# Performance work log

Hardware: AMD Instinct MI355X
Metric: run time of the kernel (lower is better)

## Reference

```python
import jax, jax.numpy as jnp
import numpy as np

PRE_NMS_THRESH = 0.05
PRE_NMS_TOP_N = 1000
NMS_THRESH = 0.6
FPN_POST_NMS_TOP_N = 100
MIN_SIZE = 0
OFFSET = 10000.0  # per-class coordinate offset for batched per-class NMS
NEG = -1e9


def bilinear_resize(x, out_h, out_w):
    # x: [H, W, C] -> [out_h, out_w, C], matches torch interpolate(align_corners=False)
    H, W, _ = x.shape
    def grid(in_size, out_size):
        scale = in_size / out_size
        src = (jnp.arange(out_size, dtype=jnp.float32) + 0.5) * scale - 0.5
        src = jnp.clip(src, 0.0, in_size - 1.0)
        i0 = jnp.floor(src).astype(jnp.int32)
        i1 = jnp.minimum(i0 + 1, in_size - 1)
        lam = src - i0.astype(jnp.float32)
        return i0, i1, lam
    r0, r1, rl = grid(H, out_h)
    c0, c1, cl = grid(W, out_w)
    x = x[r0] * (1.0 - rl)[:, None, None] + x[r1] * rl[:, None, None]
    x = x[:, c0] * (1.0 - cl)[None, :, None] + x[:, c1] * cl[None, :, None]
    return x


def box_iou_plus1(b):
    area = (b[:, 2] - b[:, 0] + 1.0) * (b[:, 3] - b[:, 1] + 1.0)
    lt = jnp.maximum(b[:, None, :2], b[None, :, :2])
    rb = jnp.minimum(b[:, None, 2:], b[None, :, 2:])
    wh = jnp.clip(rb - lt + 1.0, 0.0)
    inter = wh[..., 0] * wh[..., 1]
    union = area[:, None] + area[None, :] - inter
    return inter / jnp.maximum(union, 1e-6)


def _forward(locations, box_cls, box_regression, centerness, box_mask, h, w):
    N, C, H, W = box_cls.shape
    M2 = box_mask.shape[1]
    Mi = int(np.sqrt(M2))
    HW = H * W
    K = PRE_NMS_TOP_N

    cls = jax.nn.sigmoid(box_cls.transpose(0, 2, 3, 1).reshape(N, HW, C))
    reg = box_regression.transpose(0, 2, 3, 1).reshape(N, HW, 4)
    cent = jax.nn.sigmoid(centerness.reshape(N, HW))
    mask = jax.nn.sigmoid(box_mask.transpose(0, 2, 3, 1))  # [N,H,W,M2]

    cand = cls > PRE_NMS_THRESH               # candidates from raw cls scores
    scr = cls * cent[:, :, None]              # centerness-weighted scores

    def per_image(cand_i, scr_i, reg_i, mask_i):
        # --- threshold + per-image topk (fixed K, padded with NEG) ---
        flat = jnp.where(cand_i, scr_i, NEG).reshape(HW * C)
        vals, idx = jax.lax.top_k(flat, K)
        valid = vals > NEG / 2
        loc_idx = idx // C
        labels = idx % C + 1                  # 1-based class labels
        locs = locations[loc_idx]             # [K,2]
        r = reg_i[loc_idx]                    # [K,4]
        boxes = jnp.stack([locs[:, 0] - r[:, 0], locs[:, 1] - r[:, 1],
                           locs[:, 0] + r[:, 2], locs[:, 1] + r[:, 3]], axis=1)
        scores = jnp.sqrt(jnp.where(valid, vals, 1.0)) * valid

        # --- mask paste: mean of upsampled mask over (buggy) box region ---
        up = bilinear_resize(mask_i, h, w)                      # [h,w,M2]
        integ = jnp.pad(jnp.cumsum(jnp.cumsum(up, 0), 1), ((1, 0), (1, 0), (0, 0)))
        bi = boxes.astype(jnp.int32)          # torch .int() truncation
        x1 = jnp.maximum(bi[:, 0], 0); x2 = jnp.minimum(bi[:, 2], h - 1)
        y1 = jnp.maximum(bi[:, 1], 0); y2 = jnp.minimum(bi[:, 3], w - 1)
        # original skip condition is (x1>=x2 or y1>=x2) -- bug replicated; extra
        # y1<y2 guard avoids NaN mean over empty region
        region_ok = (x1 < x2) & (y1 < x2) & (y1 < y2)
        x1c = jnp.clip(x1, 0, h); x2c = jnp.clip(x2, 0, h)
        y1c = jnp.clip(y1, 0, w); y2c = jnp.clip(y2, 0, w)
        s = integ[x2c, y2c] - integ[x1c, y2c] - integ[x2c, y1c] + integ[x1c, y1c]
        area = jnp.maximum((x2c - x1c) * (y2c - y1c), 1).astype(s.dtype)
        prob = ((s / area[:, None]) * region_ok[:, None]).reshape(K, Mi, Mi)

        # --- clip_to_image (x in [0,w-1], y in [0,h-1]) + remove_small_boxes ---
        bx = jnp.stack([jnp.clip(boxes[:, 0], 0, w - 1), jnp.clip(boxes[:, 1], 0, h - 1),
                        jnp.clip(boxes[:, 2], 0, w - 1), jnp.clip(boxes[:, 3], 0, h - 1)], 1)
        ws_ = bx[:, 2] - bx[:, 0] + 1.0
        hs_ = bx[:, 3] - bx[:, 1] + 1.0
        valid = valid & (ws_ >= MIN_SIZE) & (hs_ >= MIN_SIZE)

        # --- per-class greedy NMS via class-offset trick (fixed shape) ---
        nb = bx + (labels.astype(bx.dtype) * OFFSET)[:, None]
        order = jnp.argsort(-jnp.where(valid, scores, -1.0))
        nb_s, sc_s, v_s = nb[order], scores[order], valid[order]
        iou = box_iou_plus1(nb_s)
        rng = jnp.arange(K)
        def step(keep, i):
            ki = keep[i] & v_s[i]
            keep = keep.at[i].set(ki)
            keep = keep & ~(ki & (iou[i] > NMS_THRESH) & (rng > i))
            return keep, None
        keep, _ = jax.lax.scan(step, jnp.ones(K, bool), jnp.arange(K))
        v_final = keep & v_s

        # --- keep fpn_post_nms_top_n highest-scoring survivors ---
        fvals, fidx = jax.lax.top_k(jnp.where(v_final, sc_s, -1.0), FPN_POST_NMS_TOP_N)
        sel = order[fidx]
        vfin = v_final[fidx]
        return (bx[sel], scores[sel] * vfin, labels[sel], prob[sel] * vfin[:, None, None], vfin)

    return jax.vmap(per_image)(cand, scr, reg, mask)


def setup_inputs() -> dict:
    key = jax.random.key(0)
    ks = jax.random.split(key, 4)
    N, C, H, W, M2 = 2, 80, 32, 40, 196
    stride = 8
    ys, xs = jnp.meshgrid(jnp.arange(H), jnp.arange(W), indexing='ij')
    locations = jnp.stack([xs.reshape(-1), ys.reshape(-1)], 1).astype(jnp.float32) * stride + stride // 2
    box_cls = jax.random.normal(ks[0], (N, C, H, W), jnp.float32) - 2.0
    box_regression = jax.random.uniform(ks[1], (N, 4, H, W), jnp.float32) * 60.0 + 4.0
    centerness = jax.random.normal(ks[2], (N, 1, H, W), jnp.float32)
    box_mask = jax.random.normal(ks[3], (N, M2, H, W), jnp.float32)
    return {"locations": locations, "box_cls": box_cls, "box_regression": box_regression,
            "centerness": centerness, "box_mask": box_mask, "image_h": 256, "image_w": 320}


def reference(locations, box_cls, box_regression, centerness, box_mask, image_h, image_w):
    return _forward(locations, box_cls, box_regression, centerness, box_mask, image_h, image_w)
```

## Files before the change

### kernel.cpp

```cpp
#include <hip/hip_runtime.h>

#define DEVI __device__ __forceinline__

constexpr int N_ = 2, C_ = 80, H_ = 32, W_ = 40, HW_ = H_ * W_, HWC_ = HW_ * C_;
constexpr int KTOP = 1000, M2_ = 196;
constexpr int IMH = 256, IMW = 320;
constexpr int BUFCAP = 4096;
constexpr int NB = 2048;
constexpr int KB = 16;
constexpr int SLICE = HWC_ / KB;

constexpr int O_SC = 800, O_LB = 1000, O_PB = 1200, O_VF = 40400;

DEVI unsigned long long mapd(double v) {
  unsigned long long u = (unsigned long long)__double_as_longlong(v);
  return (u & 0x8000000000000000ull) ? ~u : (u | 0x8000000000000000ull);
}
DEVI double unmapd(unsigned long long k) {
  unsigned long long u = (k & 0x8000000000000000ull) ? (k ^ 0x8000000000000000ull) : ~k;
  return __longlong_as_double((long long)u);
}
DEVI int binof(unsigned long long k) {
  double v = unmapd(k);
  unsigned b = __float_as_uint((float)v);
  int bin = (int)(b >> 16) - 0x3800;
  return bin < 0 ? 0 : (bin > NB - 1 ? NB - 1 : bin);
}
DEVI int i0of(int x, int cap) {
  float src = ((float)x + 0.5f) * 0.125f - 0.5f;
  src = fminf(fmaxf(src, 0.f), (float)cap);
  return (int)floorf(src);
}

__global__ __launch_bounds__(1024) void k_pre(const float* cls, const float* cent, const float* bm,
                                              unsigned long long* keys, unsigned* ghist,
                                              float* msig, float* wr, float* wc) {
  int b = blockIdx.x, tid = threadIdx.x;
  if (b < N_ * KB) {
    __shared__ unsigned hist[NB];
    __shared__ double ce[HW_];
    int n = b / KB, sb = b % KB;
    size_t base = (size_t)n * HWC_ + (size_t)sb * SLICE;
    for (int j = tid; j < NB; j += 1024) hist[j] = 0;
    for (int j = tid; j < HW_; j += 1024) ce[j] = 1.0 / (1.0 + exp(-(double)cent[n * HW_ + j]));
    __syncthreads();
    #pragma unroll
    for (int it = 0; it < 7; ++it) {
      int j = it * 1024 + tid;
      if (j < SLICE) {
        size_t t = base + j;
        int hw = j % HW_;
        double a = (double)cls[t];
        double s = 1.0 / (1.0 + exp(-a));
        double v = (s > 0.05) ? s * ce[hw] : -1e9;
        unsigned long long k = mapd(v);
        keys[t] = k;
        if (k >> 63) atomicAdd(&hist[binof(k)], 1u);
      }
    }
    __syncthreads();
    unsigned* gh = ghist + ((size_t)n * KB + sb) * NB;
    for (int j = tid; j < NB; j += 1024) gh[j] = hist[j];
  } else if (b < N_ * KB + 140) {
    __shared__ float tile[4][32][33];
    int g = tid >> 8, sub = tid & 255;
    int tt = (b - N_ * KB) * 4 + g;
    int n = tt / 280, r = tt % 280, rqt = r / 7, ct = r % 7;
    int tx = sub & 31, ty = sub >> 5;
    int rq0 = rqt * 32, c0 = ct * 32;
    for (int i = 0; i < 4; ++i) {
      int cc = c0 + ty + i * 8, rq = rq0 + tx;
      if (cc < M2_) {
        float v = bm[((size_t)n * M2_ + cc) * HW_ + rq];
        tile[g][ty + i * 8][tx] = 1.f / (1.f + expf(-v));
      }
    }
    __syncthreads();
    for (int i = 0; i < 4; ++i) {
      int rq = rq0 + ty + i * 8, cc = c0 + tx;
      if (cc < M2_) msig[((size_t)n * HW_ + rq) * M2_ + cc] = tile[g][tx][ty + i * 8];
    }
  } else {
    int t = tid;
    if (t < H_) {
      int r = t; float acc = 0.f; wr[0 * H_ + r] = 0.f;
      for (int x = 0; x < IMH; ++x) {
        float src = ((float)x + 0.5f) * ((float)H_ / (float)IMH) - 0.5f;
        src = fminf(fmaxf(src, 0.f), (float)(H_ - 1));
        int i0 = (int)floorf(src); int i1 = min(i0 + 1, H_ - 1);
        float lam = src - (float)i0;
        float w = ((r == i0) ? (1.f - lam) : 0.f) + ((r == i1) ? lam : 0.f);
        acc += w; wr[(x + 1) * H_ + r] = acc;
      }
    } else if (t < H_ + W_) {
      int q = t - H_; float acc = 0.f; wc[0 * W_ + q] = 0.f;
      for (int y = 0; y < IMW; ++y) {
        float src = ((float)y + 0.5f) * ((float)W_ / (float)IMW) - 0.5f;
        src = fminf(fmaxf(src, 0.f), (float)(W_ - 1));
        int i0 = (int)floorf(src); int i1 = min(i0 + 1, W_ - 1);
        float lam = src - (float)i0;
        float w = ((q == i0) ? (1.f - lam) : 0.f) + ((q == i1) ? lam : 0.f);
        acc += w; wc[(y + 1) * W_ + q] = acc;
      }
    }
  }
}

__global__ __launch_bounds__(1024) void k_compact(const unsigned long long* keys, const unsigned* ghist,
                                                  unsigned long long* bufK, unsigned* bufI, unsigned* cntG) {
  __shared__ unsigned wtot[16], wabove[16], sliceCnt[16], sliceOff[17];
  __shared__ unsigned sD, lcnt;
  int b = blockIdx.x, n = b >> 4, sb = b & 15;
  int tid = threadIdx.x, lane = tid & 63, wid = tid >> 6;
  const unsigned* gh = ghist + (size_t)n * KB * NB;
  unsigned a = 0, bv = 0;
  #pragma unroll
  for (int q = 0; q < KB; ++q) { a += gh[q * NB + 2 * tid]; bv += gh[q * NB + 2 * tid + 1]; }
  if (tid == 0) { sD = 0; lcnt = 0; }
  unsigned s = a + bv, suf = s;
  for (int off = 1; off < 64; off <<= 1) {
    unsigned v = __shfl_down(suf, off);
    if (lane + off < 64) suf += v;
  }
  if (lane == 0) wtot[wid] = suf;
  __syncthreads();
  if (tid == 0) { unsigned acc = 0; for (int w = 15; w >= 0; --w) { wabove[w] = acc; acc += wtot[w]; } }
  __syncthreads();
  unsigned above = (suf - s) + wabove[wid];
  if (above < 1000u && above + bv >= 1000u) sD = (unsigned)(2 * tid + 1);
  if (above + bv < 1000u && above + bv + a >= 1000u) sD = (unsigned)(2 * tid);
  __syncthreads();
  unsigned D = sD;

  {
    unsigned acc = 0;
    for (int bin = (int)D + lane; bin < NB; bin += 64) acc += gh[wid * NB + bin];
    for (int off = 32; off; off >>= 1) acc += __shfl_down(acc, off);
    if (lane == 0) sliceCnt[wid] = acc;
  }
  __syncthreads();
  if (tid == 0) {
    unsigned acc = 0;
    for (int q = 0; q < KB; ++q) { sliceOff[q] = acc; acc += sliceCnt[q]; }
    sliceOff[KB] = acc;
    if (sb == 0) cntG[n] = acc;
  }
  __syncthreads();
  unsigned myStart = sliceOff[sb];

  const unsigned long long* kb = keys + (size_t)n * HWC_ + (size_t)sb * SLICE;
  for (int it = 0; it < 7; ++it) {
    int j = it * 1024 + tid;
    bool win = false; unsigned long long k = 0;
    if (j < SLICE) { k = kb[j]; win = (k >> 63) && (unsigned)binof(k) >= D; }
    unsigned long long mb = __ballot(win);
    if (mb) {
      int lead = __builtin_ctzll(mb);
      unsigned offw = 0;
      if (lane == lead) offw = atomicAdd(&lcnt, (unsigned)__popcll(mb));
      offw = (unsigned)__shfl((int)offw, lead);
      if (win) {
        unsigned pos = myStart + offw + (unsigned)__popcll(mb & ((1ull << lane) - 1ull));
        if (pos < BUFCAP) {
          int hw = j % HW_, c = sb * 5 + j / HW_;
          bufK[(size_t)n * BUFCAP + pos] = k;
          bufI[(size_t)n * BUFCAP + pos] = (unsigned)(hw * C_ + c);
        }
      }
    }
  }
}

struct SortSh { unsigned long long K[BUFCAP]; unsigned I[BUFCAP]; };

__global__ __launch_bounds__(1024) void k_sortdec(const unsigned long long* bufK, const unsigned* bufI,
                                                  const unsigned* cntG, const float* loc, const float* breg,
                                                  double* bxd, double* scd, int* lab, int* vld, int* rg,
                                                  unsigned* keepg) {
  __shared__ SortSh sh;
  int n = blockIdx.x, tid = threadIdx.x;
  keepg[n * 1024 + tid] = 0;
  unsigned cnt = cntG[n]; if (cnt > BUFCAP) cnt = BUFCAP;
  int P = 1024; while (P < (int)cnt) P <<= 1;
  for (int j = tid; j < P; j += 1024) {
    if (j < (int)cnt) { sh.K[j] = bufK[(size_t)n * BUFCAP + j]; sh.I[j] = bufI[(size_t)n * BUFCAP + j]; }
    else { sh.K[j] = 0ull; sh.I[j] = 0xFFFFFFFFu; }
  }
  __syncthreads();
  int E = P >> 10;
  for (int sz = 2; sz <= P; sz <<= 1) {
    for (int st = sz >> 1; st >= 64; st >>= 1) {
      for (int p = tid; p < (P >> 1); p += 1024) {
        int i = ((p & ~(st - 1)) << 1) | (p & (st - 1));
        int j = i | st;
        bool up = ((i & sz) == 0);
        unsigned long long k1 = sh.K[i], k2 = sh.K[j];
        unsigned i1 = sh.I[i], i2 = sh.I[j];
        bool bef = (k1 > k2) || (k1 == k2 && i1 < i2);
        if (bef != up) { sh.K[i] = k2; sh.K[j] = k1; sh.I[i] = i2; sh.I[j] = i1; }
      }
      __syncthreads();
    }
    {
      int st0 = ((sz >> 1) < 32) ? (sz >> 1) : 32;
      for (int e = 0; e < E; ++e) {
        int elem = tid + (e << 10);
        unsigned long long k = sh.K[elem];
        unsigned ii = sh.I[elem];
        bool dir = ((elem & sz) == 0);
        for (int st = st0; st >= 1; st >>= 1) {
          unsigned long long ko = __shfl_xor(k, st);
          unsigned io = __shfl_xor(ii, st);
          bool low = ((elem & st) == 0);
          bool first = (k > ko) || (k == ko && ii < io);
          bool take_mine = first ^ (!low) ^ (!dir);
          if (!take_mine) { k = ko; ii = io; }
        }
        sh.K[elem] = k; sh.I[elem] = ii;
      }
      __syncthreads();
    }
  }

  if (tid < KTOP) {
    unsigned long long key = sh.K[tid];
    unsigned idx = sh.I[tid];
    double v = unmapd(key);
    int valid = (v > -5e8) && (idx < (unsigned)HWC_);
    if (idx >= (unsigned)HWC_) idx = 0;
    int hw = (int)(idx / C_), c = (int)(idx % C_);
    double lx = (double)loc[hw * 2 + 0], ly = (double)loc[hw * 2 + 1];
    const float* rg4 = breg + (size_t)n * 4 * HW_;
    double r0 = (double)rg4[0 * HW_ + hw], r1 = (double)rg4[1 * HW_ + hw];
    double r2 = (double)rg4[2 * HW_ + hw], r3 = (double)rg4[3 * HW_ + hw];
    double b0 = lx - r0, b1 = ly - r1, b2 = lx + r2, b3 = ly + r3;
    double sc = valid ? sqrt(v) : 0.0;
    int bi0 = (int)b0, bi1 = (int)b1, bi2 = (int)b2, bi3 = (int)b3;
    int x1 = max(bi0, 0), x2 = min(bi2, IMH - 1), y1 = max(bi1, 0), y2 = min(bi3, IMW - 1);
    int rok = (x1 < x2) && (y1 < x2) && (y1 < y2);
    int x1c = min(max(x1, 0), IMH), x2c = min(max(x2, 0), IMH);
    int y1c = min(max(y1, 0), IMW), y2c = min(max(y2, 0), IMW);
    int area = max((x2c - x1c) * (y2c - y1c), 1);
    double c0 = fmin(fmax(b0, 0.0), (double)(IMW - 1));
    double c1 = fmin(fmax(b1, 0.0), (double)(IMH - 1));
    double c2 = fmin(fmax(b2, 0.0), (double)(IMW - 1));
    double c3 = fmin(fmax(b3, 0.0), (double)(IMH - 1));
    size_t base = (size_t)n * 1024 + tid;
    bxd[base * 4 + 0] = c0; bxd[base * 4 + 1] = c1; bxd[base * 4 + 2] = c2; bxd[base * 4 + 3] = c3;
    scd[base] = sc; lab[base] = c + 1; vld[base] = valid;
    int* r8 = rg + base * 8;
    r8[0] = x1c; r8[1] = x2c; r8[2] = y1c; r8[3] = y2c; r8[4] = area; r8[5] = rok;
  }
}

__global__ void k_nms(const double* bxd, const int* lab, const int* vld, unsigned* keepg) {
  int cls = blockIdx.x + 1, n = blockIdx.y, tid = threadIdx.x;
  __shared__ int mk[KTOP];
  __shared__ double mb0[KTOP], mb1[KTOP], mb2[KTOP], mb3[KTOP], ma[KTOP];
  __shared__ unsigned char kept[KTOP];
  int m = 0;
  for (int base = 0; base < KTOP; base += 64) {
    int t = base + tid;
    bool pred = (t < KTOP) && (lab[n * 1024 + t] == cls) && (vld[n * 1024 + t] != 0);
    unsigned long long bb = __ballot(pred);
    if (pred) {
      int pos = m + (int)__popcll(bb & ((1ull << tid) - 1ull));
      mk[pos] = t;
      const double* p = bxd + ((size_t)n * 1024 + t) * 4;
      double b0 = p[0], b1 = p[1], b2 = p[2], b3 = p[3];
      mb0[pos] = b0; mb1[pos] = b1; mb2[pos] = b2; mb3[pos] = b3;
      ma[pos] = (b2 - b0 + 1.0) * (b3 - b1 + 1.0);
      kept[pos] = 1;
    }
    m += (int)__popcll(bb);
  }
  __syncthreads();
  for (int i = 0; i < m; ++i) {
    if (kept[i]) {
      double x1 = mb0[i], y1 = mb1[i], x2 = mb2[i], y2 = mb3[i], ai = ma[i];
      for (int j = i + 1 + tid; j < m; j += 64) {
        double ltx = fmax(x1, mb0[j]), lty = fmax(y1, mb1[j]);
        double rbx = fmin(x2, mb2[j]), rby = fmin(y2, mb3[j]);
        double iw = fmax(rbx - ltx + 1.0, 0.0), ih = fmax(rby - lty + 1.0, 0.0);
        double inter = iw * ih;
        double uni = ai + ma[j] - inter;
        if (inter / fmax(uni, 1e-6) > 0.6) kept[j] = 0;
      }
    }
    __syncthreads();
  }
  for (int i = tid; i < m; i += 64) keepg[n * 1024 + mk[i]] = (unsigned)kept[i];
}

__global__ __launch_bounds__(256) void k_finish(const unsigned* keepg, const double* bxd,
                                                const double* scd, const int* lab, const int* rg,
                                                const float* msig, const float* wr, const float* wc,
                                                float* out) {
  int t = blockIdx.x, n = blockIdx.y, tid = threadIdx.x, lane = tid & 63, wid = tid >> 6;
  __shared__ int lsel[100], lvf[100];
  __shared__ unsigned woff[4]; __shared__ unsigned sS;
  __shared__ float A[H_], B[W_];

  int i0 = tid * 4;
  unsigned ff[4]; int lc = 0;
  for (int j = 0; j < 4; ++j) {
    int i = i0 + j;
    ff[j] = (i < KTOP) ? keepg[n * 1024 + i] : 0u;
    lc += (int)ff[j];
  }
  unsigned pre = (unsigned)lc;
  for (int off = 1; off < 64; off <<= 1) {
    unsigned v = __shfl_up(pre, off);
    if (lane >= off) pre += v;
  }
  if (lane == 63) woff[wid] = pre;
  __syncthreads();
  if (tid == 0) { unsigned acc = 0; for (int w = 0; w < 4; ++w) { unsigned tmp = woff[w]; woff[w] = acc; acc += tmp; } sS = acc; }
  __syncthreads();
  int kpre = (int)(woff[wid] + pre - (unsigned)lc);
  int S = (int)sS;
  for (int j = 0; j < 4; ++j) {
    int i = i0 + j;
    if (i < KTOP) {
      if (ff[j]) { if (kpre < 100) { lsel[kpre] = i; lvf[kpre] = 1; } kpre++; }
      else { int slot = S + (i - kpre); if (slot < 100) { lsel[slot] = i; lvf[slot] = 0; } }
    }
  }
  __syncthreads();

  int k = lsel[t], vf = lvf[t];
  if (tid == 0) {
    const double* bb = bxd + ((size_t)n * 1024 + k) * 4;
    out[(n * 100 + t) * 4 + 0] = (float)bb[0];
    out[(n * 100 + t) * 4 + 1] = (float)bb[1];
    out[(n * 100 + t) * 4 + 2] = (float)bb[2];
    out[(n * 100 + t) * 4 + 3] = (float)bb[3];
    out[O_SC + n * 100 + t] = vf ? (float)scd[n * 1024 + k] : 0.f;
    out[O_LB + n * 100 + t] = (float)lab[n * 1024 + k];
    out[O_VF + n * 100 + t] = (float)vf;
  }
  const int* r8 = rg + ((size_t)n * 1024 + k) * 8;
  int x1c = r8[0], x2c = r8[1], y1c = r8[2], y2c = r8[3], area = r8[4], rok = r8[5];
  if (tid < H_) A[tid] = wr[x2c * H_ + tid] - wr[x1c * H_ + tid];
  else if (tid < H_ + W_) { int q = tid - H_; B[q] = wc[y2c * W_ + q] - wc[y1c * W_ + q]; }
  __syncthreads();
  if (tid < M2_) {
    float acc = 0.f;
    if (rok && vf) {
      int rlo = i0of(x1c, H_ - 1);
      int rhi = min(i0of(x2c - 1, H_ - 1) + 1, H_ - 1);
      int qlo = i0of(y1c, W_ - 1);
      int qhi = min(i0of(y2c - 1, W_ - 1) + 1, W_ - 1);
      for (int r = rlo; r <= rhi; ++r) {
        float ar = A[r];
        const float* mrow = msig + ((size_t)((n * H_ + r) * W_ + qlo)) * M2_ + tid;
        float rs = 0.f;
        #pragma unroll 4
        for (int q = qlo; q <= qhi; ++q) { rs += B[q] * mrow[0]; mrow += M2_; }
        acc += ar * rs;
      }
      acc /= (float)area;
    }
    out[O_PB + (size_t)(n * 100 + t) * M2_ + tid] = acc;
  }
}

extern "C" void kernel_launch(void* const* d_in, const int* in_sizes, int n_in,
                              void* d_out, int out_size, void* d_ws, size_t ws_size,
                              hipStream_t stream) {
  (void)in_sizes; (void)n_in; (void)out_size; (void)ws_size;
  const float* locations = (const float*)d_in[0];
  const float* box_cls   = (const float*)d_in[1];
  const float* box_reg   = (const float*)d_in[2];
  const float* cent      = (const float*)d_in[3];
  const float* box_mask  = (const float*)d_in[4];
  float* out = (float*)d_out;

  char* ws = (char*)d_ws;
  size_t off = 0;
  auto alloc = [&](size_t bytes) -> void* {
    void* p = ws + off;
    off = (off + bytes + 255) & ~(size_t)255;
    return p;
  };
  unsigned long long* keys = (unsigned long long*)alloc((size_t)N_ * HWC_ * 8);
  unsigned* ghist          = (unsigned*)alloc((size_t)N_ * KB * NB * 4);
  unsigned long long* bufK = (unsigned long long*)alloc((size_t)N_ * BUFCAP * 8);
  unsigned* bufI           = (unsigned*)alloc((size_t)N_ * BUFCAP * 4);
  unsigned* cntG           = (unsigned*)alloc(16 * 4);
  double* bxd              = (double*)alloc((size_t)N_ * 1024 * 4 * 8);
  double* scd              = (double*)alloc((size_t)N_ * 1024 * 8);
  int* lab                 = (int*)alloc((size_t)N_ * 1024 * 4);
  int* vld                 = (int*)alloc((size_t)N_ * 1024 * 4);
  int* rg                  = (int*)alloc((size_t)N_ * 1024 * 8 * 4);
  unsigned* keepg          = (unsigned*)alloc((size_t)N_ * 1024 * 4);
  float* msig              = (float*)alloc((size_t)N_ * HW_ * M2_ * 4);
  float* wr                = (float*)alloc((size_t)(IMH + 1) * H_ * 4);
  float* wc                = (float*)alloc((size_t)(IMW + 1) * W_ * 4);

  k_pre<<<N_ * KB + 140 + 1, 1024, 0, stream>>>(box_cls, cent, box_mask, keys, ghist, msig, wr, wc);
  k_compact<<<N_ * KB, 1024, 0, stream>>>(keys, ghist, bufK, bufI, cntG);
  k_sortdec<<<N_, 1024, 0, stream>>>(bufK, bufI, cntG, locations, box_reg, bxd, scd, lab, vld, rg, keepg);
  k_nms<<<dim3(C_, N_), 64, 0, stream>>>(bxd, lab, vld, keepg);
  k_finish<<<dim3(100, N_), 256, 0, stream>>>(keepg, bxd, scd, lab, rg, msig, wr, wc, out);
}
```

Measured before the change: 91.03 us.

## Bin-sort candidates in pre pass and fuse compaction into sort kernel

The pre pass now computes scores in float, records each candidate's histogram bin in shared memory, and scatters candidate indices into per-slice, bin-ordered lists. It no longer writes a full 64-bit key array. The separate compaction kernel is removed, and the sort kernel reads only the candidates in the top bins, widened by one bin to absorb float rounding, and recomputes exact double-precision keys for them. This removes one launch and the large key write and reread, in exchange for a bin-boundary approximation and extra recomputation of sigmoid in double for the selected candidates.

Measured after the change: 100.9 us. 1.11x slower.

```diff
diff --git a/kernel.cpp b/kernel.cpp
--- a/kernel.cpp
+++ b/kernel.cpp
@@ -20,12 +20,6 @@
   unsigned long long u = (k & 0x8000000000000000ull) ? (k ^ 0x8000000000000000ull) : ~k;
   return __longlong_as_double((long long)u);
 }
-DEVI int binof(unsigned long long k) {
-  double v = unmapd(k);
-  unsigned b = __float_as_uint((float)v);
-  int bin = (int)(b >> 16) - 0x3800;
-  return bin < 0 ? 0 : (bin > NB - 1 ? NB - 1 : bin);
-}
 DEVI int i0of(int x, int cap) {
   float src = ((float)x + 0.5f) * 0.125f - 0.5f;
   src = fminf(fmaxf(src, 0.f), (float)cap);
@@ -33,34 +27,68 @@
 }
 
 __global__ __launch_bounds__(1024) void k_pre(const float* cls, const float* cent, const float* bm,
-                                              unsigned long long* keys, unsigned* ghist,
+                                              unsigned* ghist, unsigned* cand,
                                               float* msig, float* wr, float* wc) {
   int b = blockIdx.x, tid = threadIdx.x;
   if (b < N_ * KB) {
     __shared__ unsigned hist[NB];
-    __shared__ double ce[HW_];
+    __shared__ unsigned run[NB];
+    __shared__ unsigned short binls[SLICE];
+    __shared__ float ce[HW_];
+    __shared__ unsigned wtot[16], wabove[16];
     int n = b / KB, sb = b % KB;
     size_t base = (size_t)n * HWC_ + (size_t)sb * SLICE;
     for (int j = tid; j < NB; j += 1024) hist[j] = 0;
-    for (int j = tid; j < HW_; j += 1024) ce[j] = 1.0 / (1.0 + exp(-(double)cent[n * HW_ + j]));
+    for (int j = tid; j < HW_; j += 1024) ce[j] = 1.f / (1.f + expf(-cent[n * HW_ + j]));
     __syncthreads();
     #pragma unroll
     for (int it = 0; it < 7; ++it) {
       int j = it * 1024 + tid;
       if (j < SLICE) {
-        size_t t = base + j;
-        int hw = j % HW_;
-        double a = (double)cls[t];
-        double s = 1.0 / (1.0 + exp(-a));
-        double v = (s > 0.05) ? s * ce[hw] : -1e9;
-        unsigned long long k = mapd(v);
-        keys[t] = k;
-        if (k >> 63) atomicAdd(&hist[binof(k)], 1u);
+        float a = cls[base + j];
+        float s = 1.f / (1.f + expf(-a));
+        unsigned short bb = 0xFFFF;
+        if (s > 0.0499999f) {
+          float key = s * ce[j % HW_];
+          unsigned kb2 = __float_as_uint(key);
+          int bin = (int)(kb2 >> 16) - 0x3800;
+          bin = bin < 0 ? 0 : (bin > NB - 1 ? NB - 1 : bin);
+          bb = (unsigned short)bin;
+          atomicAdd(&hist[bin], 1u);
+        }
+        binls[j] = bb;
       }
     }
     __syncthreads();
     unsigned* gh = ghist + ((size_t)n * KB + sb) * NB;
     for (int j = tid; j < NB; j += 1024) gh[j] = hist[j];
+    int lane = tid & 63, wid = tid >> 6;
+    unsigned aa = hist[2 * tid], bv = hist[2 * tid + 1];
+    unsigned s2 = aa + bv, suf = s2;
+    for (int off = 1; off < 64; off <<= 1) {
+      unsigned v = __shfl_down(suf, off);
+      if (lane + off < 64) suf += v;
+    }
+    if (lane == 0) wtot[wid] = suf;
+    __syncthreads();
+    if (tid == 0) { unsigned acc = 0; for (int w = 15; w >= 0; --w) { wabove[w] = acc; acc += wtot[w]; } }
+    __syncthreads();
+    unsigned above = (suf - s2) + wabove[wid];
+    run[2 * tid + 1] = above;
+    run[2 * tid] = above + bv;
+    __syncthreads();
+    unsigned* ca = cand + ((size_t)n * KB + sb) * SLICE;
+    #pragma unroll
+    for (int it = 0; it < 7; ++it) {
+      int j = it * 1024 + tid;
+      if (j < SLICE) {
+        unsigned short bb = binls[j];
+        if (bb != 0xFFFF) {
+          unsigned pos = atomicAdd(&run[bb], 1u);
+          ca[pos] = (unsigned)(base + j);
+        }
+      }
+    }
   } else if (b < N_ * KB + 140) {
     __shared__ float tile[4][32][33];
     int g = tid >> 8, sub = tid & 255;
@@ -106,18 +134,24 @@
   }
 }
 
-__global__ __launch_bounds__(1024) void k_compact(const unsigned long long* keys, const unsigned* ghist,
-                                                  unsigned long long* bufK, unsigned* bufI, unsigned* cntG) {
+struct SortSh { unsigned long long K[BUFCAP]; unsigned I[BUFCAP]; };
+
+__global__ __launch_bounds__(1024) void k_sel(const unsigned* ghist, const unsigned* cand,
+                                              const float* cls, const float* cent,
+                                              const float* loc, const float* breg,
+                                              double* bxd, double* scd, int* lab, int* vld, int* rg,
+                                              unsigned* keepg) {
+  __shared__ SortSh sh;
   __shared__ unsigned wtot[16], wabove[16], sliceCnt[16], sliceOff[17];
-  __shared__ unsigned sD, lcnt;
-  int b = blockIdx.x, n = b >> 4, sb = b & 15;
-  int tid = threadIdx.x, lane = tid & 63, wid = tid >> 6;
+  __shared__ unsigned sD;
+  int n = blockIdx.x, tid = threadIdx.x, lane = tid & 63, wid = tid >> 6;
+  keepg[n * 1024 + tid] = 0;
   const unsigned* gh = ghist + (size_t)n * KB * NB;
   unsigned a = 0, bv = 0;
   #pragma unroll
   for (int q = 0; q < KB; ++q) { a += gh[q * NB + 2 * tid]; bv += gh[q * NB + 2 * tid + 1]; }
-  if (tid == 0) { sD = 0; lcnt = 0; }
-  unsigned s = a + bv, suf = s;
+  if (tid == 0) sD = 0;
+  unsigned s2 = a + bv, suf = s2;
   for (int off = 1; off < 64; off <<= 1) {
     unsigned v = __shfl_down(suf, off);
     if (lane + off < 64) suf += v;
@@ -126,15 +160,15 @@
   __syncthreads();
   if (tid == 0) { unsigned acc = 0; for (int w = 15; w >= 0; --w) { wabove[w] = acc; acc += wtot[w]; } }
   __syncthreads();
-  unsigned above = (suf - s) + wabove[wid];
+  unsigned above = (suf - s2) + wabove[wid];
   if (above < 1000u && above + bv >= 1000u) sD = (unsigned)(2 * tid + 1);
   if (above + bv < 1000u && above + bv + a >= 1000u) sD = (unsigned)(2 * tid);
   __syncthreads();
   unsigned D = sD;
-
+  unsigned Dg = (D > 0) ? D - 1 : 0;
   {
     unsigned acc = 0;
-    for (int bin = (int)D + lane; bin < NB; bin += 64) acc += gh[wid * NB + bin];
+    for (int bin = (int)Dg + lane; bin < NB; bin += 64) acc += gh[wid * NB + bin];
     for (int off = 32; off; off >>= 1) acc += __shfl_down(acc, off);
     if (lane == 0) sliceCnt[wid] = acc;
   }
@@ -143,49 +177,30 @@
     unsigned acc = 0;
     for (int q = 0; q < KB; ++q) { sliceOff[q] = acc; acc += sliceCnt[q]; }
     sliceOff[KB] = acc;
-    if (sb == 0) cntG[n] = acc;
-  }
-  __syncthreads();
-  unsigned myStart = sliceOff[sb];
-
-  const unsigned long long* kb = keys + (size_t)n * HWC_ + (size_t)sb * SLICE;
-  for (int it = 0; it < 7; ++it) {
-    int j = it * 1024 + tid;
-    bool win = false; unsigned long long k = 0;
-    if (j < SLICE) { k = kb[j]; win = (k >> 63) && (unsigned)binof(k) >= D; }
-    unsigned long long mb = __ballot(win);
-    if (mb) {
-      int lead = __builtin_ctzll(mb);
-      unsigned offw = 0;
-      if (lane == lead) offw = atomicAdd(&lcnt, (unsigned)__popcll(mb));
-      offw = (unsigned)__shfl((int)offw, lead);
-      if (win) {
-        unsigned pos = myStart + offw + (unsigned)__popcll(mb & ((1ull << lane) - 1ull));
-        if (pos < BUFCAP) {
-          int hw = j % HW_, c = sb * 5 + j / HW_;
-          bufK[(size_t)n * BUFCAP + pos] = k;
-          bufI[(size_t)n * BUFCAP + pos] = (unsigned)(hw * C_ + c);
-        }
-      }
-    }
-  }
-}
-
-struct SortSh { unsigned long long K[BUFCAP]; unsigned I[BUFCAP]; };
-
-__global__ __launch_bounds__(1024) void k_sortdec(const unsigned long long* bufK, const unsigned* bufI,
-                                                  const unsigned* cntG, const float* loc, const float* breg,
-                                                  double* bxd, double* scd, int* lab, int* vld, int* rg,
-                                                  unsigned* keepg) {
-  __shared__ SortSh sh;
-  int n = blockIdx.x, tid = threadIdx.x;
-  keepg[n * 1024 + tid] = 0;
-  unsigned cnt = cntG[n]; if (cnt > BUFCAP) cnt = BUFCAP;
-  int P = 1024; while (P < (int)cnt) P <<= 1;
-  for (int j = tid; j < P; j += 1024) {
-    if (j < (int)cnt) { sh.K[j] = bufK[(size_t)n * BUFCAP + j]; sh.I[j] = bufI[(size_t)n * BUFCAP + j]; }
-    else { sh.K[j] = 0ull; sh.I[j] = 0xFFFFFFFFu; }
-  }
+  }
+  __syncthreads();
+  int G = (int)sliceOff[KB]; if (G > BUFCAP) G = BUFCAP;
+  {
+    const unsigned* ca = cand + ((size_t)n * KB + wid) * SLICE;
+    unsigned cs = sliceCnt[wid], so = sliceOff[wid];
+    for (unsigned e = lane; e < cs; e += 64) {
+      unsigned pos = so + e;
+      if (pos < (unsigned)BUFCAP) {
+        unsigned t = ca[e];
+        int c = (int)((t % (unsigned)HWC_) / (unsigned)HW_);
+        int hw = (int)(t % (unsigned)HW_);
+        double aa = (double)cls[t];
+        double ss = 1.0 / (1.0 + exp(-aa));
+        double ced = 1.0 / (1.0 + exp(-(double)cent[n * HW_ + hw]));
+        double v = (ss > 0.05) ? ss * ced : -1e9;
+        sh.K[pos] = mapd(v);
+        sh.I[pos] = (unsigned)(hw * C_ + c);
+      }
+    }
+  }
+  __syncthreads();
+  int P = 1024; while (P < G) P <<= 1;
+  for (int j = G + tid; j < P; j += 1024) { sh.K[j] = 0ull; sh.I[j] = 0xFFFFFFFFu; }
   __syncthreads();
   int E = P >> 10;
   for (int sz = 2; sz <= P; sz <<= 1) {
@@ -383,24 +398,21 @@
     off = (off + bytes + 255) & ~(size_t)255;
     return p;
   };
-  unsigned long long* keys = (unsigned long long*)alloc((size_t)N_ * HWC_ * 8);
-  unsigned* ghist          = (unsigned*)alloc((size_t)N_ * KB * NB * 4);
-  unsigned long long* bufK = (unsigned long long*)alloc((size_t)N_ * BUFCAP * 8);
-  unsigned* bufI           = (unsigned*)alloc((size_t)N_ * BUFCAP * 4);
-  unsigned* cntG           = (unsigned*)alloc(16 * 4);
-  double* bxd              = (double*)alloc((size_t)N_ * 1024 * 4 * 8);
-  double* scd              = (double*)alloc((size_t)N_ * 1024 * 8);
-  int* lab                 = (int*)alloc((size_t)N_ * 1024 * 4);
-  int* vld                 = (int*)alloc((size_t)N_ * 1024 * 4);
-  int* rg                  = (int*)alloc((size_t)N_ * 1024 * 8 * 4);
-  unsigned* keepg          = (unsigned*)alloc((size_t)N_ * 1024 * 4);
-  float* msig              = (float*)alloc((size_t)N_ * HW_ * M2_ * 4);
-  float* wr                = (float*)alloc((size_t)(IMH + 1) * H_ * 4);
-  float* wc                = (float*)alloc((size_t)(IMW + 1) * W_ * 4);
-
-  k_pre<<<N_ * KB + 140 + 1, 1024, 0, stream>>>(box_cls, cent, box_mask, keys, ghist, msig, wr, wc);
-  k_compact<<<N_ * KB, 1024, 0, stream>>>(keys, ghist, bufK, bufI, cntG);
-  k_sortdec<<<N_, 1024, 0, stream>>>(bufK, bufI, cntG, locations, box_reg, bxd, scd, lab, vld, rg, keepg);
+  unsigned* ghist = (unsigned*)alloc((size_t)N_ * KB * NB * 4);
+  unsigned* cand  = (unsigned*)alloc((size_t)N_ * KB * SLICE * 4);
+  double* bxd     = (double*)alloc((size_t)N_ * 1024 * 4 * 8);
+  double* scd     = (double*)alloc((size_t)N_ * 1024 * 8);
+  int* lab        = (int*)alloc((size_t)N_ * 1024 * 4);
+  int* vld        = (int*)alloc((size_t)N_ * 1024 * 4);
+  int* rg         = (int*)alloc((size_t)N_ * 1024 * 8 * 4);
+  unsigned* keepg = (unsigned*)alloc((size_t)N_ * 1024 * 4);
+  float* msig     = (float*)alloc((size_t)N_ * HW_ * M2_ * 4);
+  float* wr       = (float*)alloc((size_t)(IMH + 1) * H_ * 4);
+  float* wc       = (float*)alloc((size_t)(IMW + 1) * W_ * 4);
+
+  k_pre<<<N_ * KB + 140 + 1, 1024, 0, stream>>>(box_cls, cent, box_mask, ghist, cand, msig, wr, wc);
+  k_sel<<<N_, 1024, 0, stream>>>(ghist, cand, box_cls, cent, locations, box_reg,
+                                 bxd, scd, lab, vld, rg, keepg);
   k_nms<<<dim3(C_, N_), 64, 0, stream>>>(bxd, lab, vld, keepg);
   k_finish<<<dim3(100, N_), 256, 0, stream>>>(keepg, bxd, scd, lab, rg, msig, wr, wc, out);
 }
```

## Recompute scores in fp32 instead of storing keys; replace bitonic sort with bucket rank

Applied to the files above, without the earlier changes.

Drops the global per-element 64-bit key buffer. The histogram and compaction kernels now recompute sigmoid scores in float, and double precision is evaluated only for the selected candidates. The full bitonic sort over up to 4096 elements in shared memory is replaced by a histogram bucket scatter followed by within-bucket rank counting, which writes the top 1024 directly. The compaction threshold is lowered by one bin to absorb float versus double binning differences. This adds a buffer-capacity cap of 2048 and a risk of mis-ranking near bin boundaries.

Result: no change. 91.70 us (+0.7%).

```diff
diff --git a/kernel.cpp b/kernel.cpp
--- a/kernel.cpp
+++ b/kernel.cpp
@@ -5,10 +5,11 @@
 constexpr int N_ = 2, C_ = 80, H_ = 32, W_ = 40, HW_ = H_ * W_, HWC_ = HW_ * C_;
 constexpr int KTOP = 1000, M2_ = 196;
 constexpr int IMH = 256, IMW = 320;
-constexpr int BUFCAP = 4096;
 constexpr int NB = 2048;
 constexpr int KB = 16;
 constexpr int SLICE = HWC_ / KB;
+constexpr int BCAP = 2048;
+constexpr int GCAP = 4096;
 
 constexpr int O_SC = 800, O_LB = 1000, O_PB = 1200, O_VF = 40400;
 
@@ -19,12 +20,6 @@
 DEVI double unmapd(unsigned long long k) {
   unsigned long long u = (k & 0x8000000000000000ull) ? (k ^ 0x8000000000000000ull) : ~k;
   return __longlong_as_double((long long)u);
-}
-DEVI int binof(unsigned long long k) {
-  double v = unmapd(k);
-  unsigned b = __float_as_uint((float)v);
-  int bin = (int)(b >> 16) - 0x3800;
-  return bin < 0 ? 0 : (bin > NB - 1 ? NB - 1 : bin);
 }
 DEVI int i0of(int x, int cap) {
   float src = ((float)x + 0.5f) * 0.125f - 0.5f;
@@ -33,29 +28,28 @@
 }
 
 __global__ __launch_bounds__(1024) void k_pre(const float* cls, const float* cent, const float* bm,
-                                              unsigned long long* keys, unsigned* ghist,
-                                              float* msig, float* wr, float* wc) {
+                                              unsigned* ghist, float* msig, float* wr, float* wc) {
   int b = blockIdx.x, tid = threadIdx.x;
   if (b < N_ * KB) {
     __shared__ unsigned hist[NB];
-    __shared__ double ce[HW_];
-    int n = b / KB, sb = b % KB;
+    __shared__ float ce[HW_];
+    int n = b >> 4, sb = b & 15;
     size_t base = (size_t)n * HWC_ + (size_t)sb * SLICE;
     for (int j = tid; j < NB; j += 1024) hist[j] = 0;
-    for (int j = tid; j < HW_; j += 1024) ce[j] = 1.0 / (1.0 + exp(-(double)cent[n * HW_ + j]));
+    for (int j = tid; j < HW_; j += 1024) ce[j] = 1.f / (1.f + expf(-cent[n * HW_ + j]));
     __syncthreads();
     #pragma unroll
     for (int it = 0; it < 7; ++it) {
       int j = it * 1024 + tid;
       if (j < SLICE) {
-        size_t t = base + j;
-        int hw = j % HW_;
-        double a = (double)cls[t];
-        double s = 1.0 / (1.0 + exp(-a));
-        double v = (s > 0.05) ? s * ce[hw] : -1e9;
-        unsigned long long k = mapd(v);
-        keys[t] = k;
-        if (k >> 63) atomicAdd(&hist[binof(k)], 1u);
+        float aa = cls[base + j];
+        float s = 1.f / (1.f + expf(-aa));
+        if (s > 0.0499999f) {
+          unsigned key = __float_as_uint(s * ce[j % HW_]);
+          int bin = (int)(key >> 16) - 0x3800;
+          bin = bin < 0 ? 0 : (bin > NB - 1 ? NB - 1 : bin);
+          atomicAdd(&hist[bin], 1u);
+        }
       }
     }
     __syncthreads();
@@ -106,18 +100,20 @@
   }
 }
 
-__global__ __launch_bounds__(1024) void k_compact(const unsigned long long* keys, const unsigned* ghist,
+__global__ __launch_bounds__(1024) void k_compact(const unsigned* ghist, const float* cls, const float* cent,
                                                   unsigned long long* bufK, unsigned* bufI, unsigned* cntG) {
   __shared__ unsigned wtot[16], wabove[16], sliceCnt[16], sliceOff[17];
   __shared__ unsigned sD, lcnt;
+  __shared__ float ce[HW_];
   int b = blockIdx.x, n = b >> 4, sb = b & 15;
   int tid = threadIdx.x, lane = tid & 63, wid = tid >> 6;
+  for (int j = tid; j < HW_; j += 1024) ce[j] = 1.f / (1.f + expf(-cent[n * HW_ + j]));
   const unsigned* gh = ghist + (size_t)n * KB * NB;
   unsigned a = 0, bv = 0;
   #pragma unroll
   for (int q = 0; q < KB; ++q) { a += gh[q * NB + 2 * tid]; bv += gh[q * NB + 2 * tid + 1]; }
   if (tid == 0) { sD = 0; lcnt = 0; }
-  unsigned s = a + bv, suf = s;
+  unsigned s2 = a + bv, suf = s2;
   for (int off = 1; off < 64; off <<= 1) {
     unsigned v = __shfl_down(suf, off);
     if (lane + off < 64) suf += v;
@@ -126,15 +122,15 @@
   __syncthreads();
   if (tid == 0) { unsigned acc = 0; for (int w = 15; w >= 0; --w) { wabove[w] = acc; acc += wtot[w]; } }
   __syncthreads();
-  unsigned above = (suf - s) + wabove[wid];
+  unsigned above = (suf - s2) + wabove[wid];
   if (above < 1000u && above + bv >= 1000u) sD = (unsigned)(2 * tid + 1);
   if (above + bv < 1000u && above + bv + a >= 1000u) sD = (unsigned)(2 * tid);
   __syncthreads();
   unsigned D = sD;
-
+  unsigned Dg = (D > 0) ? D - 1 : 0;
   {
     unsigned acc = 0;
-    for (int bin = (int)D + lane; bin < NB; bin += 64) acc += gh[wid * NB + bin];
+    for (int bin = (int)Dg + lane; bin < NB; bin += 64) acc += gh[wid * NB + bin];
     for (int off = 32; off; off >>= 1) acc += __shfl_down(acc, off);
     if (lane == 0) sliceCnt[wid] = acc;
   }
@@ -147,12 +143,20 @@
   }
   __syncthreads();
   unsigned myStart = sliceOff[sb];
-
-  const unsigned long long* kb = keys + (size_t)n * HWC_ + (size_t)sb * SLICE;
+  size_t gbase = (size_t)n * HWC_ + (size_t)sb * SLICE;
   for (int it = 0; it < 7; ++it) {
     int j = it * 1024 + tid;
-    bool win = false; unsigned long long k = 0;
-    if (j < SLICE) { k = kb[j]; win = (k >> 63) && (unsigned)binof(k) >= D; }
+    bool win = false; float aa = 0.f;
+    if (j < SLICE) {
+      aa = cls[gbase + j];
+      float s = 1.f / (1.f + expf(-aa));
+      if (s > 0.0499999f) {
+        unsigned key = __float_as_uint(s * ce[j % HW_]);
+        int bin = (int)(key >> 16) - 0x3800;
+        bin = bin < 0 ? 0 : (bin > NB - 1 ? NB - 1 : bin);
+        win = ((unsigned)bin >= Dg);
+      }
+    }
     unsigned long long mb = __ballot(win);
     if (mb) {
       int lead = __builtin_ctzll(mb);
@@ -161,70 +165,94 @@
       offw = (unsigned)__shfl((int)offw, lead);
       if (win) {
         unsigned pos = myStart + offw + (unsigned)__popcll(mb & ((1ull << lane) - 1ull));
-        if (pos < BUFCAP) {
+        if (pos < (unsigned)GCAP) {
           int hw = j % HW_, c = sb * 5 + j / HW_;
-          bufK[(size_t)n * BUFCAP + pos] = k;
-          bufI[(size_t)n * BUFCAP + pos] = (unsigned)(hw * C_ + c);
+          double ss = 1.0 / (1.0 + exp(-(double)aa));
+          double ced = 1.0 / (1.0 + exp(-(double)cent[n * HW_ + hw]));
+          double v = (ss > 0.05) ? ss * ced : -1e9;
+          bufK[(size_t)n * GCAP + pos] = mapd(v);
+          bufI[(size_t)n * GCAP + pos] = (unsigned)(hw * C_ + c);
         }
       }
     }
   }
 }
 
-struct SortSh { unsigned long long K[BUFCAP]; unsigned I[BUFCAP]; };
-
-__global__ __launch_bounds__(1024) void k_sortdec(const unsigned long long* bufK, const unsigned* bufI,
+struct RankSh {
+  unsigned long long K[BCAP];
+  unsigned I[BCAP];
+  unsigned short eb[BCAP];
+  unsigned short ord[BCAP];
+  unsigned bh[NB], bs[NB], cur[NB];
+  unsigned long long Ks[1024];
+  unsigned Is[1024];
+  unsigned wtot[16], wabove[16];
+};
+
+__global__ __launch_bounds__(1024) void k_rankdec(const unsigned long long* bufK, const unsigned* bufI,
                                                   const unsigned* cntG, const float* loc, const float* breg,
                                                   double* bxd, double* scd, int* lab, int* vld, int* rg,
                                                   unsigned* keepg) {
-  __shared__ SortSh sh;
-  int n = blockIdx.x, tid = threadIdx.x;
+  __shared__ RankSh sh;
+  int n = blockIdx.x, tid = threadIdx.x, lane = tid & 63, wid = tid >> 6;
   keepg[n * 1024 + tid] = 0;
-  unsigned cnt = cntG[n]; if (cnt > BUFCAP) cnt = BUFCAP;
-  int P = 1024; while (P < (int)cnt) P <<= 1;
-  for (int j = tid; j < P; j += 1024) {
-    if (j < (int)cnt) { sh.K[j] = bufK[(size_t)n * BUFCAP + j]; sh.I[j] = bufI[(size_t)n * BUFCAP + j]; }
-    else { sh.K[j] = 0ull; sh.I[j] = 0xFFFFFFFFu; }
-  }
-  __syncthreads();
-  int E = P >> 10;
-  for (int sz = 2; sz <= P; sz <<= 1) {
-    for (int st = sz >> 1; st >= 64; st >>= 1) {
-      for (int p = tid; p < (P >> 1); p += 1024) {
-        int i = ((p & ~(st - 1)) << 1) | (p & (st - 1));
-        int j = i | st;
-        bool up = ((i & sz) == 0);
-        unsigned long long k1 = sh.K[i], k2 = sh.K[j];
-        unsigned i1 = sh.I[i], i2 = sh.I[j];
-        bool bef = (k1 > k2) || (k1 == k2 && i1 < i2);
-        if (bef != up) { sh.K[i] = k2; sh.K[j] = k1; sh.I[i] = i2; sh.I[j] = i1; }
-      }
-      __syncthreads();
-    }
-    {
-      int st0 = ((sz >> 1) < 32) ? (sz >> 1) : 32;
-      for (int e = 0; e < E; ++e) {
-        int elem = tid + (e << 10);
-        unsigned long long k = sh.K[elem];
-        unsigned ii = sh.I[elem];
-        bool dir = ((elem & sz) == 0);
-        for (int st = st0; st >= 1; st >>= 1) {
-          unsigned long long ko = __shfl_xor(k, st);
-          unsigned io = __shfl_xor(ii, st);
-          bool low = ((elem & st) == 0);
-          bool first = (k > ko) || (k == ko && ii < io);
-          bool take_mine = first ^ (!low) ^ (!dir);
-          if (!take_mine) { k = ko; ii = io; }
-        }
-        sh.K[elem] = k; sh.I[elem] = ii;
-      }
-      __syncthreads();
-    }
-  }
-
+  int G = (int)cntG[n]; if (G > BCAP) G = BCAP;
+  for (int j = tid; j < NB; j += 1024) sh.bh[j] = 0;
+  for (int p = tid; p < G; p += 1024) {
+    sh.K[p] = bufK[(size_t)n * GCAP + p];
+    sh.I[p] = bufI[(size_t)n * GCAP + p];
+  }
+  __syncthreads();
+  for (int p = tid; p < G; p += 1024) {
+    double v = unmapd(sh.K[p]);
+    int bb = 0;
+    if (v > 0.0) {
+      unsigned kb = __float_as_uint((float)v);
+      bb = (int)(kb >> 16) - 0x3800;
+      bb = bb < 0 ? 0 : (bb > NB - 1 ? NB - 1 : bb);
+    }
+    sh.eb[p] = (unsigned short)bb;
+    atomicAdd(&sh.bh[bb], 1u);
+  }
+  __syncthreads();
+  {
+    unsigned a2 = sh.bh[2 * tid], b2 = sh.bh[2 * tid + 1];
+    unsigned s3 = a2 + b2, suf2 = s3;
+    for (int off = 1; off < 64; off <<= 1) {
+      unsigned v = __shfl_down(suf2, off);
+      if (lane + off < 64) suf2 += v;
+    }
+    if (lane == 0) sh.wtot[wid] = suf2;
+    __syncthreads();
+    if (tid == 0) { unsigned acc = 0; for (int w = 15; w >= 0; --w) { sh.wabove[w] = acc; acc += sh.wtot[w]; } }
+    __syncthreads();
+    unsigned above2 = (suf2 - s3) + sh.wabove[wid];
+    sh.bs[2 * tid + 1] = above2;  sh.cur[2 * tid + 1] = above2;
+    sh.bs[2 * tid] = above2 + b2; sh.cur[2 * tid] = above2 + b2;
+  }
+  __syncthreads();
+  for (int p = tid; p < G; p += 1024) {
+    unsigned p2 = atomicAdd(&sh.cur[sh.eb[p]], 1u);
+    sh.ord[p2] = (unsigned short)p;
+  }
+  __syncthreads();
+  for (int p = tid; p < G; p += 1024) {
+    int bb = sh.eb[p];
+    unsigned lo = sh.bs[bb], len = sh.bh[bb];
+    unsigned long long k1 = sh.K[p]; unsigned i1 = sh.I[p];
+    unsigned r = lo;
+    for (unsigned q = lo; q < lo + len; ++q) {
+      int j = sh.ord[q];
+      unsigned long long kj = sh.K[j]; unsigned ij = sh.I[j];
+      if ((kj > k1) || (kj == k1 && ij < i1)) ++r;
+    }
+    if (r < 1024u) { sh.Ks[r] = k1; sh.Is[r] = i1; }
+  }
+  for (int j = G + tid; j < 1024; j += 1024) { sh.Ks[j] = 0ull; sh.Is[j] = 0xFFFFFFFFu; }
+  __syncthreads();
   if (tid < KTOP) {
-    unsigned long long key = sh.K[tid];
-    unsigned idx = sh.I[tid];
+    unsigned long long key = sh.Ks[tid];
+    unsigned idx = sh.Is[tid];
     double v = unmapd(key);
     int valid = (v > -5e8) && (idx < (unsigned)HWC_);
     if (idx >= (unsigned)HWC_) idx = 0;
@@ -383,10 +411,9 @@
     off = (off + bytes + 255) & ~(size_t)255;
     return p;
   };
-  unsigned long long* keys = (unsigned long long*)alloc((size_t)N_ * HWC_ * 8);
   unsigned* ghist          = (unsigned*)alloc((size_t)N_ * KB * NB * 4);
-  unsigned long long* bufK = (unsigned long long*)alloc((size_t)N_ * BUFCAP * 8);
-  unsigned* bufI           = (unsigned*)alloc((size_t)N_ * BUFCAP * 4);
+  unsigned long long* bufK = (unsigned long long*)alloc((size_t)N_ * GCAP * 8);
+  unsigned* bufI           = (unsigned*)alloc((size_t)N_ * GCAP * 4);
   unsigned* cntG           = (unsigned*)alloc(16 * 4);
   double* bxd              = (double*)alloc((size_t)N_ * 1024 * 4 * 8);
   double* scd              = (double*)alloc((size_t)N_ * 1024 * 8);
@@ -398,9 +425,10 @@
   float* wr                = (float*)alloc((size_t)(IMH + 1) * H_ * 4);
   float* wc                = (float*)alloc((size_t)(IMW + 1) * W_ * 4);
 
-  k_pre<<<N_ * KB + 140 + 1, 1024, 0, stream>>>(box_cls, cent, box_mask, keys, ghist, msig, wr, wc);
-  k_compact<<<N_ * KB, 1024, 0, stream>>>(keys, ghist, bufK, bufI, cntG);
-  k_sortdec<<<N_, 1024, 0, stream>>>(bufK, bufI, cntG, locations, box_reg, bxd, scd, lab, vld, rg, keepg);
+  k_pre<<<N_ * KB + 140 + 1, 1024, 0, stream>>>(box_cls, cent, box_mask, ghist, msig, wr, wc);
+  k_compact<<<N_ * KB, 1024, 0, stream>>>(ghist, box_cls, cent, bufK, bufI, cntG);
+  k_rankdec<<<N_, 1024, 0, stream>>>(bufK, bufI, cntG, locations, box_reg,
+                                     bxd, scd, lab, vld, rg, keepg);
   k_nms<<<dim3(C_, N_), 64, 0, stream>>>(bxd, lab, vld, keepg);
   k_finish<<<dim3(100, N_), 256, 0, stream>>>(keepg, bxd, scd, lab, rg, msig, wr, wc, out);
 }
```
